# Performance work log

Measured on AMD Instinct MI355X. Metric: run time of the kernel, lower is better.

The kernel has to match this reference:

```python
import jax, jax.numpy as jnp
import numpy as np

B, S, E, H = 64, 512, 1024, 1024

def setup_inputs() -> dict:
    key = jax.random.key(0)
    k1, k2, k3, k4, k5 = jax.random.split(key, 5)
    emben_x = jax.random.normal(k1, (B, S, E), dtype=jnp.float32)
    sW = 1.0 / np.sqrt(E)
    sU = 1.0 / np.sqrt(H)
    W_w = jax.random.uniform(k2, (H, E), jnp.float32, -sW, sW)
    W_b = jax.random.uniform(k3, (H,), jnp.float32, -sW, sW)
    U_w = jax.random.uniform(k4, (H, H), jnp.float32, -sU, sU)
    U_b = jax.random.uniform(k5, (H,), jnp.float32, -sU, sU)
    return {"emben_x": emben_x, "W_w": W_w, "W_b": W_b, "U_w": U_w, "U_b": U_b}

def reference(emben_x, W_w, W_b, U_w, U_b):
    # Precompute input projection for all timesteps in one big GEMM: [B,S,H]
    wx = jnp.einsum('bse,he->bsh', emben_x, W_w) + W_b

    def step(t, wx_t):
        # h3 = tanh(W x_t + b_W + t); t_new = U h3 + b_U
        h3 = jnp.tanh(wx_t + t)
        t_new = h3 @ U_w.T + U_b
        return t_new, t_new

    t0 = jnp.zeros((emben_x.shape[0], U_w.shape[0]), dtype=emben_x.dtype)
    t_final, outs = jax.lax.scan(step, t0, jnp.swapaxes(wx, 0, 1))  # outs: [S,B,H]
    result1 = jnp.swapaxes(outs, 0, 1)  # [B,S,H]
    return result1, t_final
```

## Files before the change

kernel.cpp:

```cpp
#include <hip/hip_runtime.h>
#include <hip/hip_bf16.h>
#include <math.h>

#define RB 64
#define RS 512
#define RE 1024
#define RH 1024
#define BSH ((size_t)RB * RS * RH)

#define NBLK 256

typedef __attribute__((ext_vector_type(8))) __bf16 bf16x8;
typedef __attribute__((ext_vector_type(4))) float  f32x4;

__device__ __forceinline__ bf16x8 cvt8(f32x4 a, f32x4 b) {
    bf16x8 r;
    r[0] = (__bf16)a[0]; r[1] = (__bf16)a[1];
    r[2] = (__bf16)a[2]; r[3] = (__bf16)a[3];
    r[4] = (__bf16)b[0]; r[5] = (__bf16)b[1];
    r[6] = (__bf16)b[2]; r[7] = (__bf16)b[3];
    return r;
}

__device__ __forceinline__ bf16x8 ld_frag_agent(const unsigned long long* p) {
    union { unsigned long long u[2]; bf16x8 v; } r;
    r.u[0] = __hip_atomic_load(p,     __ATOMIC_RELAXED, __HIP_MEMORY_SCOPE_AGENT);
    r.u[1] = __hip_atomic_load(p + 1, __ATOMIC_RELAXED, __HIP_MEMORY_SCOPE_AGENT);
    return r.v;
}
__device__ __forceinline__ void st_bf16_agent(__bf16* p, float v) {
    union { __bf16 b; unsigned short s; } u;
    u.b = (__bf16)v;
    __hip_atomic_store(reinterpret_cast<unsigned short*>(p), u.s,
                       __ATOMIC_RELAXED, __HIP_MEMORY_SCOPE_AGENT);
}

__global__ void init_flags_k(unsigned* sync) {
    if (threadIdx.x < 256) sync[threadIdx.x] = 0u;
}

#define WBK  64
#define LDST 72

__global__ __launch_bounds__(256) void wx_gemm(
    const float* __restrict__ X,
    const float* __restrict__ Ww,
    const float* __restrict__ Wb,
    float* __restrict__ Out)
{
    __shared__ __align__(16) __bf16 As[128 * LDST];
    __shared__ __align__(16) __bf16 Bs[128 * LDST];

    const int tid  = threadIdx.x;
    const int lane = tid & 63;
    const int wave = tid >> 6;
    const int m0   = blockIdx.y * 128;
    const int n0   = blockIdx.x * 128;
    const int wm   = (wave >> 1) * 64;
    const int wn   = (wave & 1) * 64;

    const int sk   = (tid & 7) * 8;
    const int srow = tid >> 3;

    f32x4 acc[4][4];
#pragma unroll
    for (int i = 0; i < 4; ++i)
#pragma unroll
        for (int j = 0; j < 4; ++j) acc[i][j] = (f32x4){0.f, 0.f, 0.f, 0.f};

    for (int kc = 0; kc < RE; kc += WBK) {
#pragma unroll
        for (int rr = 0; rr < 128; rr += 32) {
            const float* xp = X + (size_t)(m0 + srow + rr) * RE + kc + sk;
            *reinterpret_cast<bf16x8*>(&As[(srow + rr) * LDST + sk]) =
                cvt8(*reinterpret_cast<const f32x4*>(xp),
                     *reinterpret_cast<const f32x4*>(xp + 4));
            const float* wp = Ww + (size_t)(n0 + srow + rr) * RE + kc + sk;
            *reinterpret_cast<bf16x8*>(&Bs[(srow + rr) * LDST + sk]) =
                cvt8(*reinterpret_cast<const f32x4*>(wp),
                     *reinterpret_cast<const f32x4*>(wp + 4));
        }
        __syncthreads();

#pragma unroll
        for (int ks = 0; ks < 2; ++ks) {
            bf16x8 af[4], bfr[4];
#pragma unroll
            for (int i = 0; i < 4; ++i) {
                af[i]  = *reinterpret_cast<const bf16x8*>(
                    &As[(wm + i * 16 + (lane & 15)) * LDST + ks * 32 + (lane >> 4) * 8]);
                bfr[i] = *reinterpret_cast<const bf16x8*>(
                    &Bs[(wn + i * 16 + (lane & 15)) * LDST + ks * 32 + (lane >> 4) * 8]);
            }
#pragma unroll
            for (int i = 0; i < 4; ++i)
#pragma unroll
                for (int j = 0; j < 4; ++j)
                    acc[i][j] = __builtin_amdgcn_mfma_f32_16x16x32_bf16(
                        af[i], bfr[j], acc[i][j], 0, 0, 0);
        }
        __syncthreads();
    }

    const int col = lane & 15, rbase = (lane >> 4) * 4;
#pragma unroll
    for (int j = 0; j < 4; ++j) {
        const int n = n0 + wn + j * 16 + col;
        const float bias = Wb[n];
#pragma unroll
        for (int i = 0; i < 4; ++i) {
#pragma unroll
            for (int r = 0; r < 4; ++r) {
                const int m = m0 + wm + i * 16 + rbase + r;
                Out[(size_t)m * RH + n] = acc[i][j][r] + bias;
            }
        }
    }
}

__device__ __forceinline__ void gbar_rg(unsigned* sync, unsigned g, int tid, int rg)
{
    __syncthreads();
    if (tid == 0) {
        unsigned old = __hip_atomic_fetch_add(&sync[rg * 32], 1u,
                                              __ATOMIC_RELAXED, __HIP_MEMORY_SCOPE_AGENT);
        if (old == 64u * g - 1u) {
            __hip_atomic_store(&sync[128 + rg * 32], g,
                               __ATOMIC_RELAXED, __HIP_MEMORY_SCOPE_AGENT);
        } else {
            while (__hip_atomic_load(&sync[128 + rg * 32],
                                     __ATOMIC_RELAXED, __HIP_MEMORY_SCOPE_AGENT) < g)
                __builtin_amdgcn_s_sleep(2);
        }
    }
    __syncthreads();
}

__global__ __launch_bounds__(256) void rnn_scan(
    const float* __restrict__ Uw,
    const float* __restrict__ Ub,
    float* Out,
    __bf16* hbuf,
    unsigned* sync)
{
    __shared__ float red[4 * 256];
    __shared__ float ubs[16];

    const int tid  = threadIdx.x;
    const int lane = tid & 63;
    const int wave = tid >> 6;
    const int bid  = blockIdx.x;
    const int cg   = bid >> 2;
    const int rg   = bid & 3;
    const int col0 = cg * 16;
    const int row0 = rg * 16;

    bf16x8 ufr[8];
    {
        const float* up = Uw + (size_t)(col0 + (lane & 15)) * RH
                        + 256 * wave + ((lane >> 4) * 8);
#pragma unroll
        for (int j = 0; j < 8; ++j)
            ufr[j] = cvt8(*reinterpret_cast<const f32x4*>(up + j * 32),
                          *reinterpret_cast<const f32x4*>(up + j * 32 + 4));
    }
    if (tid < 16) ubs[tid] = Ub[col0 + tid];

    const int erow = row0 + (tid >> 4);
    const int ecol = col0 + (tid & 15);

    st_bf16_agent(hbuf + erow * RH + ecol,
                  tanhf(Out[(size_t)erow * RS * RH + ecol]));
    gbar_rg(sync, 1u, tid, rg);

    const int arow  = row0 + (lane & 15);
    const int kbase = 256 * wave + (lane >> 4) * 8;

    for (int t = 0; t < RS; ++t) {
        const __bf16* cur = hbuf + (size_t)(t & 1) * (RB * RH);
        __bf16*       nxt = hbuf + (size_t)((t + 1) & 1) * (RB * RH);
        const unsigned long long* cp =
            reinterpret_cast<const unsigned long long*>(cur)
            + ((size_t)arow * RH + kbase) / 4;

        bf16x8 x0 = ld_frag_agent(cp + 0 * 8);
        bf16x8 x1 = ld_frag_agent(cp + 1 * 8);
        bf16x8 x2 = ld_frag_agent(cp + 2 * 8);
        bf16x8 x3 = ld_frag_agent(cp + 3 * 8);
        bf16x8 x4 = ld_frag_agent(cp + 4 * 8);
        bf16x8 x5 = ld_frag_agent(cp + 5 * 8);
        bf16x8 x6 = ld_frag_agent(cp + 6 * 8);
        bf16x8 x7 = ld_frag_agent(cp + 7 * 8);

        float wn = 0.f;
        if (t < RS - 1)
            wn = Out[(size_t)erow * RS * RH + (size_t)(t + 1) * RH + ecol];

        f32x4 ac0 = (f32x4){0.f, 0.f, 0.f, 0.f};
        f32x4 ac1 = ac0, ac2 = ac0, ac3 = ac0;
        ac0 = __builtin_amdgcn_mfma_f32_16x16x32_bf16(x0, ufr[0], ac0, 0, 0, 0);
        ac1 = __builtin_amdgcn_mfma_f32_16x16x32_bf16(x1, ufr[1], ac1, 0, 0, 0);
        ac2 = __builtin_amdgcn_mfma_f32_16x16x32_bf16(x2, ufr[2], ac2, 0, 0, 0);
        ac3 = __builtin_amdgcn_mfma_f32_16x16x32_bf16(x3, ufr[3], ac3, 0, 0, 0);
        ac0 = __builtin_amdgcn_mfma_f32_16x16x32_bf16(x4, ufr[4], ac0, 0, 0, 0);
        ac1 = __builtin_amdgcn_mfma_f32_16x16x32_bf16(x5, ufr[5], ac1, 0, 0, 0);
        ac2 = __builtin_amdgcn_mfma_f32_16x16x32_bf16(x6, ufr[6], ac2, 0, 0, 0);
        ac3 = __builtin_amdgcn_mfma_f32_16x16x32_bf16(x7, ufr[7], ac3, 0, 0, 0);
        const f32x4 acc = (ac0 + ac1) + (ac2 + ac3);

#pragma unroll
        for (int r = 0; r < 4; ++r)
            red[wave * 256 + ((lane >> 4) * 4 + r) * 16 + (lane & 15)] = acc[r];
        __syncthreads();

        const float v = red[tid] + red[256 + tid] + red[512 + tid] + red[768 + tid]
                      + ubs[tid & 15];
        const size_t oidx = (size_t)erow * RS * RH + (size_t)t * RH + ecol;
        Out[oidx] = v;
        if (t == RS - 1) {
            Out[BSH + (size_t)erow * RH + ecol] = v;
        } else {
            st_bf16_agent(nxt + erow * RH + ecol, tanhf(wn + v));
            gbar_rg(sync, (unsigned)(t + 2), tid, rg);
        }
    }
}

extern "C" void kernel_launch(void* const* d_in, const int* in_sizes, int n_in,
                              void* d_out, int out_size, void* d_ws, size_t ws_size,
                              hipStream_t stream)
{
    const float* X  = (const float*)d_in[0];
    const float* Ww = (const float*)d_in[1];
    const float* Wb = (const float*)d_in[2];
    const float* Uw = (const float*)d_in[3];
    const float* Ub = (const float*)d_in[4];
    float* Out = (float*)d_out;

    __bf16* hbuf = (__bf16*)d_ws;
    unsigned* sync = (unsigned*)((char*)d_ws + (size_t)2 * RB * RH * sizeof(__bf16));

    hipLaunchKernelGGL(init_flags_k, dim3(1), dim3(256), 0, stream, sync);
    hipLaunchKernelGGL(wx_gemm, dim3(RH / 128, (RB * RS) / 128), dim3(256), 0, stream,
                       X, Ww, Wb, Out);
    hipLaunchKernelGGL(rnn_scan, dim3(NBLK), dim3(256), 0, stream,
                       Uw, Ub, Out, hbuf, sync);
}
```

Measured before the change: 2.271 ms.

## Replace counter barrier with per-block flags polled by a whole wave

Swaps the per-row-group atomic counter barrier (fetch_add plus a release store that one thread spins on) for per-block step flags. Each block publishes its step number, and one wave of the consumer polls all 64 producer flags in its row group with a wave-wide vote. This removes the serialized atomic increment and the two-hop release, so a block can start as soon as its producers finish. The next timestep's wx value is also prefetched one step earlier, and the Out store is moved after the h store, to shorten the critical path. The risk is extra polling traffic on the flags, and ordering now rests on relaxed atomics plus a __syncthreads before each flag store.

```diff
diff --git a/kernel.cpp b/kernel.cpp
--- a/kernel.cpp
+++ b/kernel.cpp
@@ -35,8 +35,8 @@
                        __ATOMIC_RELAXED, __HIP_MEMORY_SCOPE_AGENT);
 }
 
-__global__ void init_flags_k(unsigned* sync) {
-    if (threadIdx.x < 256) sync[threadIdx.x] = 0u;
+__global__ void init_flags_k(unsigned* flags) {
+    if (threadIdx.x < NBLK) flags[threadIdx.x] = 0u;
 }
 
 #define WBK  64
@@ -118,30 +118,12 @@
     }
 }
 
-__device__ __forceinline__ void gbar_rg(unsigned* sync, unsigned g, int tid, int rg)
-{
-    __syncthreads();
-    if (tid == 0) {
-        unsigned old = __hip_atomic_fetch_add(&sync[rg * 32], 1u,
-                                              __ATOMIC_RELAXED, __HIP_MEMORY_SCOPE_AGENT);
-        if (old == 64u * g - 1u) {
-            __hip_atomic_store(&sync[128 + rg * 32], g,
-                               __ATOMIC_RELAXED, __HIP_MEMORY_SCOPE_AGENT);
-        } else {
-            while (__hip_atomic_load(&sync[128 + rg * 32],
-                                     __ATOMIC_RELAXED, __HIP_MEMORY_SCOPE_AGENT) < g)
-                __builtin_amdgcn_s_sleep(2);
-        }
-    }
-    __syncthreads();
-}
-
 __global__ __launch_bounds__(256) void rnn_scan(
     const float* __restrict__ Uw,
     const float* __restrict__ Ub,
     float* Out,
     __bf16* hbuf,
-    unsigned* sync)
+    unsigned* flags)
 {
     __shared__ float red[4 * 256];
     __shared__ float ubs[16];
@@ -154,6 +136,7 @@
     const int rg   = bid & 3;
     const int col0 = cg * 16;
     const int row0 = rg * 16;
+    const int slot = rg * 64 + cg;
 
     bf16x8 ufr[8];
     {
@@ -171,10 +154,15 @@
 
     st_bf16_agent(hbuf + erow * RH + ecol,
                   tanhf(Out[(size_t)erow * RS * RH + ecol]));
-    gbar_rg(sync, 1u, tid, rg);
+    float wn_cur = Out[(size_t)erow * RS * RH + (size_t)1 * RH + ecol];
+    __syncthreads();
+    if (tid == 0)
+        __hip_atomic_store(&flags[slot], 1u,
+                           __ATOMIC_RELAXED, __HIP_MEMORY_SCOPE_AGENT);
 
     const int arow  = row0 + (lane & 15);
     const int kbase = 256 * wave + (lane >> 4) * 8;
+    const unsigned* myflags = flags + rg * 64;
 
     for (int t = 0; t < RS; ++t) {
         const __bf16* cur = hbuf + (size_t)(t & 1) * (RB * RH);
@@ -182,6 +170,17 @@
         const unsigned long long* cp =
             reinterpret_cast<const unsigned long long*>(cur)
             + ((size_t)arow * RH + kbase) / 4;
+
+        const unsigned tgt = (unsigned)(t + 1);
+        while (true) {
+            const unsigned f = __hip_atomic_load(&myflags[lane],
+                                                 __ATOMIC_RELAXED,
+                                                 __HIP_MEMORY_SCOPE_AGENT);
+            if (__all(f >= tgt)) break;
+            __builtin_amdgcn_s_sleep(1);
+        }
+        __builtin_amdgcn_sched_barrier(0);
+        asm volatile("" ::: "memory");
 
         bf16x8 x0 = ld_frag_agent(cp + 0 * 8);
         bf16x8 x1 = ld_frag_agent(cp + 1 * 8);
@@ -191,10 +190,6 @@
         bf16x8 x5 = ld_frag_agent(cp + 5 * 8);
         bf16x8 x6 = ld_frag_agent(cp + 6 * 8);
         bf16x8 x7 = ld_frag_agent(cp + 7 * 8);
-
-        float wn = 0.f;
-        if (t < RS - 1)
-            wn = Out[(size_t)erow * RS * RH + (size_t)(t + 1) * RH + ecol];
 
         f32x4 ac0 = (f32x4){0.f, 0.f, 0.f, 0.f};
         f32x4 ac1 = ac0, ac2 = ac0, ac3 = ac0;
@@ -216,12 +211,18 @@
         const float v = red[tid] + red[256 + tid] + red[512 + tid] + red[768 + tid]
                       + ubs[tid & 15];
         const size_t oidx = (size_t)erow * RS * RH + (size_t)t * RH + ecol;
-        Out[oidx] = v;
         if (t == RS - 1) {
+            Out[oidx] = v;
             Out[BSH + (size_t)erow * RH + ecol] = v;
         } else {
-            st_bf16_agent(nxt + erow * RH + ecol, tanhf(wn + v));
-            gbar_rg(sync, (unsigned)(t + 2), tid, rg);
+            st_bf16_agent(nxt + erow * RH + ecol, tanhf(wn_cur + v));
+            Out[oidx] = v;
+            if (t < RS - 2)
+                wn_cur = Out[(size_t)erow * RS * RH + (size_t)(t + 2) * RH + ecol];
+            __syncthreads();
+            if (tid == 0)
+                __hip_atomic_store(&flags[slot], (unsigned)(t + 2),
+                                   __ATOMIC_RELAXED, __HIP_MEMORY_SCOPE_AGENT);
         }
     }
 }
@@ -238,11 +239,11 @@
     float* Out = (float*)d_out;
 
     __bf16* hbuf = (__bf16*)d_ws;
-    unsigned* sync = (unsigned*)((char*)d_ws + (size_t)2 * RB * RH * sizeof(__bf16));
-
-    hipLaunchKernelGGL(init_flags_k, dim3(1), dim3(256), 0, stream, sync);
+    unsigned* flags = (unsigned*)((char*)d_ws + (size_t)2 * RB * RH * sizeof(__bf16));
+
+    hipLaunchKernelGGL(init_flags_k, dim3(1), dim3(256), 0, stream, flags);
     hipLaunchKernelGGL(wx_gemm, dim3(RH / 128, (RB * RS) / 128), dim3(256), 0, stream,
                        X, Ww, Wb, Out);
     hipLaunchKernelGGL(rnn_scan, dim3(NBLK), dim3(256), 0, stream,
-                       Uw, Ub, Out, hbuf, sync);
-}
+                       Uw, Ub, Out, hbuf, flags);
+}
```

Measured after the change: 2.242 ms. Within noise of the previous version (-1.3%).
